# Kernel tuning notes

Measured on AMD Instinct MI355X. Metric: run time of the kernel, lower is better.

## Reference

```python
import jax, jax.numpy as jnp
import numpy as np

G, S, F, H, C, L = 32, 2048, 128, 128, 40, 3
N = G * S           # 65536 nodes
E = N * 16          # 1048576 edges


def setup_inputs() -> dict:
    key = jax.random.key(0)
    ks = jax.random.split(key, 10)
    x = jax.random.normal(ks[0], (N, F), dtype=jnp.float32)
    edge_index = jax.random.randint(ks[1], (2, E), 0, N, dtype=jnp.int64)
    E_meta = jax.random.normal(ks[2], (G, H), dtype=jnp.float32)
    ptr = (jnp.arange(G + 1, dtype=jnp.int64) * S)  # uniform partitions
    # learned params (xavier-ish scaling)
    w0 = jax.random.normal(ks[3], (F, 1), dtype=jnp.float32) * (2.0 / (F + 1)) ** 0.5
    b0 = jax.random.normal(ks[4], (F, H), dtype=jnp.float32) * (2.0 / (F + H)) ** 0.5
    conv_w = jax.random.normal(ks[5], (L, H, H), dtype=jnp.float32) * (1.0 / H) ** 0.5
    conv_b = jnp.zeros((L, H), dtype=jnp.float32)
    lt1_w = jax.random.normal(ks[6], (C, H), dtype=jnp.float32) * (1.0 / H) ** 0.5
    lt1_b = jnp.zeros((C,), dtype=jnp.float32)
    return {"x": x, "edge_index": edge_index, "E_meta": E_meta, "ptr": ptr,
            "w0": w0, "b0": b0, "conv_w": conv_w, "conv_b": conv_b,
            "lt1_w": lt1_w, "lt1_b": lt1_b}


def _gcn_conv(h, src, dst, deg_inv_sqrt, W, b):
    # GCNConv (PyG defaults): h' = D^-1/2 (A+I) D^-1/2 (h W) + b
    hw = h @ W                                          # [N,H]
    norm = deg_inv_sqrt[src] * deg_inv_sqrt[dst]        # [E+N]
    msg = hw[src] * norm[:, None]                       # gather + scale
    return jax.ops.segment_sum(msg, dst, num_segments=h.shape[0]) + b


def reference(x, edge_index, E_meta, ptr, w0, b0, conv_w, conv_b, lt1_w, lt1_b):
    n_nodes = x.shape[0]
    g = E_meta.shape[0]
    s = n_nodes // g  # uniform ptr (ptr[i] = i*s) by construction
    # per-partition dynamic weight: relu(w0 @ emb^T + b0) -> [G,F,H]
    Wdyn = jax.nn.relu(w0[None, :, :] * E_meta[:, None, :] + b0[None, :, :])
    # segment matmul x[ptr[i]:ptr[i+1]] @ Wdyn[i], concatenated -> [N,H]
    h = jnp.einsum('gsf,gfh->gsh', x.reshape(g, s, -1), Wdyn).reshape(n_nodes, -1)
    # add self loops once; symmetric normalization on target degree
    loop = jnp.arange(n_nodes, dtype=edge_index.dtype)
    src = jnp.concatenate([edge_index[0], loop])
    dst = jnp.concatenate([edge_index[1], loop])
    deg = jax.ops.segment_sum(jnp.ones_like(dst, dtype=h.dtype), dst,
                              num_segments=n_nodes)
    deg_inv_sqrt = jnp.where(deg > 0, jax.lax.rsqrt(deg), 0.0)
    for l in range(conv_w.shape[0]):
        h = jax.nn.relu(_gcn_conv(h, src, dst, deg_inv_sqrt, conv_w[l], conv_b[l]))
        # F.dropout with training=False is identity (eval mode)
    logits = h @ lt1_w.T + lt1_b
    return jax.nn.log_softmax(logits, axis=1)
```

## Files before the change

### kernel.cpp

```cpp
#include <hip/hip_runtime.h>

#define NNODES 65536
#define NEDGES 1048576
#define HDIM 128
#define NCLS 40
#define BCAP 6144

#define FP8_SCALE 32.0f
#define FP8_INV   0.03125f

typedef unsigned int uint;
typedef __attribute__((ext_vector_type(8))) short bf16x8;
typedef __attribute__((ext_vector_type(4))) float f32x4;
typedef __attribute__((ext_vector_type(2))) float f32x2;

__device__ __forceinline__ float bf_lo(uint v) {
    return __builtin_bit_cast(float, v << 16);
}
__device__ __forceinline__ float bf_hi(uint v) {
    return __builtin_bit_cast(float, v & 0xffff0000u);
}
__device__ __forceinline__ uint pack_bf16x2(float a, float b) {
    uint ua = __builtin_bit_cast(uint, a);
    uint ub = __builtin_bit_cast(uint, b);
    ua += 0x7fff + ((ua >> 16) & 1);
    ub += 0x7fff + ((ub >> 16) & 1);
    return (ua >> 16) | (ub & 0xffff0000u);
}
__device__ __forceinline__ float tobf(float v) {
    uint u = __builtin_bit_cast(uint, v);
    u += 0x7fff + ((u >> 16) & 1);
    return __builtin_bit_cast(float, u & 0xffff0000u);
}

__device__ __forceinline__ f32x2 fp8_pair(uint u) {
    return __builtin_amdgcn_cvt_pk_f32_fp8((int)u, false);
}

__global__ __launch_bounds__(256) void convT_kernel(
    const float* __restrict__ cw, uint* __restrict__ WT, int* __restrict__ gcursor,
    const float* __restrict__ ltw, uint* __restrict__ WcT8)
{
    int t = threadIdx.x;
    if (blockIdx.x == 0) gcursor[t] = 0;
    int idx = blockIdx.x * 256 + t;
    if (idx < 24576) {
        int ip = idx & 63;
        int o = (idx >> 6) & 127;
        int l = idx >> 13;
        int i0 = ip * 2;
        float v0 = cw[l * 16384 + i0 * 128 + o];
        float v1 = cw[l * 16384 + (i0 + 1) * 128 + o];
        WT[idx] = pack_bf16x2(v0, v1);
    } else {
        int idx2 = idx - 24576;
        int part = (idx2 >= 3072) ? 1 : 0;
        int r = idx2 - part * 3072;
        int o = r >> 6;
        int ip = r & 63;
        float v0 = 0.f, v1 = 0.f;
        if (o < NCLS) {
            float w0v = ltw[o * 128 + ip * 2];
            float w1v = ltw[o * 128 + ip * 2 + 1];
            float h0 = tobf(w0v), h1 = tobf(w1v);
            if (part == 0) { v0 = h0; v1 = h1; }
            else { v0 = w0v - h0; v1 = w1v - h1; }
        }
        WcT8[idx2] = pack_bf16x2(v0, v1);
    }
}

__global__ __launch_bounds__(256) void bucket_scatter(
    const int* __restrict__ src, const int* __restrict__ dst,
    int* __restrict__ gcursor, uint* __restrict__ binned)
{
    __shared__ int lcnt[256];
    __shared__ int lbase[256];
    int t = threadIdx.x;
    int base = blockIdx.x * 4096;
    lcnt[t] = 0;
    __syncthreads();
    uint e[16];
#pragma unroll
    for (int k = 0; k < 16; k++) {
        int i = base + k * 256 + t;
        uint s = (uint)src[i];
        uint d = (uint)dst[i];
        e[k] = (d << 16) | s;
        atomicAdd(&lcnt[d >> 8], 1);
    }
    __syncthreads();
    lbase[t] = t * BCAP + atomicAdd(&gcursor[t], lcnt[t]);
    lcnt[t] = 0;
    __syncthreads();
#pragma unroll
    for (int k = 0; k < 16; k++) {
        int b = e[k] >> 24;
        int r = atomicAdd(&lcnt[b], 1);
        binned[lbase[b] + r] = e[k];
    }
}

__global__ __launch_bounds__(256) void prep_kernel(
    const uint* __restrict__ binned, const int* __restrict__ gcursor,
    int* __restrict__ row_beg, int* __restrict__ row_end4,
    float* __restrict__ dis, int* __restrict__ csr,
    const float* __restrict__ w0, const float* __restrict__ em,
    const float* __restrict__ b0, const uint* __restrict__ convwT0,
    uint* __restrict__ WT)
{
    __shared__ int cnt[256];
    __shared__ int tmp[256];
    __shared__ int fb[256];
    const int t = threadIdx.x;

    if (blockIdx.x < 256) {
        int b = blockIdx.x;
        int e0 = b * BCAP, e1 = e0 + gcursor[b];
        cnt[t] = 0;
        __syncthreads();
        for (int i = e0 + t; i < e1; i += 256)
            atomicAdd(&cnt[(binned[i] >> 16) & 255], 1);
        __syncthreads();
        int v = cnt[t];
        int size4 = (v + 3) & ~3;
        tmp[t] = size4;
        __syncthreads();
        for (int off = 1; off < 256; off <<= 1) {
            int u = (t >= off) ? tmp[t - off] : 0;
            __syncthreads();
            tmp[t] += u;
            __syncthreads();
        }
        fb[t] = tmp[t] - size4;
        int node = (b << 8) + t;
        int beg = e0 + fb[t];
        row_beg[node] = beg;
        row_end4[node] = beg + size4;
        dis[node] = rsqrtf((float)(v + 1));
        for (int p = v; p < size4; p++) csr[beg + p] = NNODES;
        cnt[t] = 0;
        __syncthreads();
        for (int i = e0 + t; i < e1; i += 256) {
            uint e = binned[i];
            int d = (e >> 16) & 255;
            int r = atomicAdd(&cnt[d], 1);
            csr[e0 + fb[d] + r] = (int)(e & 0xffffu);
        }
    } else {
        int bb = blockIdx.x - 256;
        const int g = bb >> 3;
        const int c = bb & 7;
        const int wave = t >> 6;
        const int lane = t & 63;
        const int q = lane >> 4;
        const int l16 = lane & 15;
        const float* emg = em + g * 128;

        f32x4 acc[2];
#pragma unroll
        for (int r = 0; r < 2; r++) {
            acc[r][0] = 0.f; acc[r][1] = 0.f; acc[r][2] = 0.f; acc[r][3] = 0.f;
        }
        const int f = c * 16 + l16;
        const float wf = w0[f];

#pragma unroll
        for (int k0 = 0; k0 < 128; k0 += 32) {
            const int kf = k0 + q * 8;
            bf16x8 afrag[2];
#pragma unroll
            for (int r = 0; r < 2; r++) {
                uint4 u = *(const uint4*)(convwT0 +
                    (size_t)(wave * 32 + r * 16 + l16) * 64 + (kf >> 1));
                afrag[r] = __builtin_bit_cast(bf16x8, u);
            }
            float4 e0 = *(const float4*)(emg + kf);
            float4 e1 = *(const float4*)(emg + kf + 4);
            const float* bp = b0 + (size_t)f * 128 + kf;
            float4 bb0 = *(const float4*)bp;
            float4 bb1 = *(const float4*)(bp + 4);
            float v0 = fmaxf(fmaf(wf, e0.x, bb0.x), 0.f);
            float v1 = fmaxf(fmaf(wf, e0.y, bb0.y), 0.f);
            float v2 = fmaxf(fmaf(wf, e0.z, bb0.z), 0.f);
            float v3 = fmaxf(fmaf(wf, e0.w, bb0.w), 0.f);
            float v4 = fmaxf(fmaf(wf, e1.x, bb1.x), 0.f);
            float v5 = fmaxf(fmaf(wf, e1.y, bb1.y), 0.f);
            float v6 = fmaxf(fmaf(wf, e1.z, bb1.z), 0.f);
            float v7 = fmaxf(fmaf(wf, e1.w, bb1.w), 0.f);
            uint4 u;
            u.x = pack_bf16x2(v0, v1);
            u.y = pack_bf16x2(v2, v3);
            u.z = pack_bf16x2(v4, v5);
            u.w = pack_bf16x2(v6, v7);
            bf16x8 bfrag = __builtin_bit_cast(bf16x8, u);
#pragma unroll
            for (int r = 0; r < 2; r++)
                acc[r] = __builtin_amdgcn_mfma_f32_16x16x32_bf16(
                    afrag[r], bfrag, acc[r], 0, 0, 0);
        }

        uint* WTg = WT + (size_t)g * 8192;
#pragma unroll
        for (int r = 0; r < 2; r++) {
            int o0 = wave * 32 + r * 16 + q * 4;
#pragma unroll
            for (int i = 0; i < 4; i++) {
                int o = o0 + i;
                float v = acc[r][i];
                float w = __shfl_xor(v, 1);
                uint p = (lane & 1) ? pack_bf16x2(w, v) : pack_bf16x2(v, w);
                if (!(lane & 1))
                    WTg[(size_t)o * 64 + (uint)(f >> 1)] = p;
            }
        }
    }
}

__device__ __forceinline__ void store_fp8_row(
    uint* __restrict__ Cp8, int row, float s32, const f32x4* accRC,
    int lane, int l16, int i)
{
#pragma unroll
    for (int c = 0; c < 8; c++) {
        float v = accRC[c][i] * s32;
        float w = __shfl_xor(v, 1);
        int us = __builtin_amdgcn_cvt_pk_fp8_f32(v, w, 0, false);
        uint partner = (uint)__shfl_xor(us, 2);
        if ((lane & 3) == 0) {
            uint p = ((uint)us & 0xffffu) | (partner << 16);
            Cp8[(size_t)row * 32 + c * 4 + (l16 >> 2)] = p;
        }
    }
}

__global__ __launch_bounds__(256) void gemm_mfma(
    const float* __restrict__ A, const uint* __restrict__ BT,
    uint* __restrict__ Cp8, const float* __restrict__ dis, int perGroup)
{
    const int t = threadIdx.x;
    const int wave = t >> 6;
    const int lane = t & 63;
    const int q = lane >> 4;
    const int l16 = lane & 15;
    const int rowBase = blockIdx.x * 128;
    const uint* Bp = perGroup ? BT + ((size_t)(rowBase >> 11) << 13) : BT;

    if (blockIdx.x == 0 && t < 32)
        Cp8[(size_t)NNODES * 32 + t] = 0u;

    f32x4 acc[2][8];
#pragma unroll
    for (int r = 0; r < 2; r++)
#pragma unroll
        for (int c = 0; c < 8; c++) {
            acc[r][c][0] = 0.f; acc[r][c][1] = 0.f;
            acc[r][c][2] = 0.f; acc[r][c][3] = 0.f;
        }

    const int mBase = rowBase + wave * 32 + l16;

#pragma unroll
    for (int k0 = 0; k0 < 128; k0 += 32) {
        const int kf = k0 + q * 8;
        bf16x8 afrag[2];
#pragma unroll
        for (int r = 0; r < 2; r++) {
            const float* ap = A + (size_t)(mBase + r * 16) * 128 + kf;
            float4 a0 = *(const float4*)ap;
            float4 a1 = *(const float4*)(ap + 4);
            uint4 u;
            u.x = pack_bf16x2(a0.x, a0.y);
            u.y = pack_bf16x2(a0.z, a0.w);
            u.z = pack_bf16x2(a1.x, a1.y);
            u.w = pack_bf16x2(a1.z, a1.w);
            afrag[r] = __builtin_bit_cast(bf16x8, u);
        }
#pragma unroll
        for (int c = 0; c < 8; c++) {
            uint4 u = *(const uint4*)(Bp + (size_t)(c * 16 + l16) * 64 + (kf >> 1));
            bf16x8 bfrag = __builtin_bit_cast(bf16x8, u);
#pragma unroll
            for (int r = 0; r < 2; r++)
                acc[r][c] = __builtin_amdgcn_mfma_f32_16x16x32_bf16(
                    afrag[r], bfrag, acc[r][c], 0, 0, 0);
        }
    }

#pragma unroll
    for (int r = 0; r < 2; r++) {
        int row0 = rowBase + wave * 32 + r * 16 + q * 4;
#pragma unroll
        for (int i = 0; i < 4; i++) {
            int row = row0 + i;
            float s32 = dis[row] * FP8_SCALE;
            store_fp8_row(Cp8, row, s32, acc[r], lane, l16, i);
        }
    }
}

__device__ __forceinline__ void aggregate_eighth(
    const uint* __restrict__ hws8_in, const int* __restrict__ row_beg,
    const int* __restrict__ row_end4, const int* __restrict__ csr,
    const float* __restrict__ dis, const float* __restrict__ bias,
    uint* __restrict__ hT, int rowBase, int wave, int lane)
{
    const int g = lane >> 3;
    const int s = lane & 7;
    const int nl = wave * 8 + g;
    const int n = rowBase + nl;
    const int beg = row_beg[n];
    const int end4 = row_end4[n];
    int mx = (end4 - beg) >> 2;
    mx = max(mx, __shfl_xor(mx, 8));
    mx = max(mx, __shfl_xor(mx, 16));
    mx = max(mx, __shfl_xor(mx, 32));

    uint4 su = *((const uint4*)(hws8_in + (size_t)n * 32) + s);
    f32x2 a[8];
    a[0] = fp8_pair(su.x); a[1] = fp8_pair(su.x >> 16);
    a[2] = fp8_pair(su.y); a[3] = fp8_pair(su.y >> 16);
    a[4] = fp8_pair(su.z); a[5] = fp8_pair(su.z >> 16);
    a[6] = fp8_pair(su.w); a[7] = fp8_pair(su.w >> 16);

#define ACC8(u) do { \
        a[0] += fp8_pair((u).x); a[1] += fp8_pair((u).x >> 16); \
        a[2] += fp8_pair((u).y); a[3] += fp8_pair((u).y >> 16); \
        a[4] += fp8_pair((u).z); a[5] += fp8_pair((u).z >> 16); \
        a[6] += fp8_pair((u).w); a[7] += fp8_pair((u).w >> 16); } while (0)

    int i = beg;
    for (int it = 0; it < mx; it += 2, i += 8) {
        int4 sA = *(const int4*)(csr + i);
        int4 sB = *(const int4*)(csr + i + 4);
        if (i >= end4) { sA.x = NNODES; sA.y = NNODES; sA.z = NNODES; sA.w = NNODES; }
        if (i + 4 >= end4) { sB.x = NNODES; sB.y = NNODES; sB.z = NNODES; sB.w = NNODES; }
        uint4 u0 = *((const uint4*)(hws8_in + (size_t)sA.x * 32) + s);
        uint4 u1 = *((const uint4*)(hws8_in + (size_t)sA.y * 32) + s);
        uint4 u2 = *((const uint4*)(hws8_in + (size_t)sA.z * 32) + s);
        uint4 u3 = *((const uint4*)(hws8_in + (size_t)sA.w * 32) + s);
        uint4 u4 = *((const uint4*)(hws8_in + (size_t)sB.x * 32) + s);
        uint4 u5 = *((const uint4*)(hws8_in + (size_t)sB.y * 32) + s);
        uint4 u6 = *((const uint4*)(hws8_in + (size_t)sB.z * 32) + s);
        uint4 u7 = *((const uint4*)(hws8_in + (size_t)sB.w * 32) + s);
        ACC8(u0); ACC8(u1); ACC8(u2); ACC8(u3);
        ACC8(u4); ACC8(u5); ACC8(u6); ACC8(u7);
    }
#undef ACC8

    const float d = dis[n] * FP8_INV;
    const float* bp = bias + s * 16;
    float4 b0 = *(const float4*)bp;
    float4 b1 = *(const float4*)(bp + 4);
    float4 b2 = *(const float4*)(bp + 8);
    float4 b3 = *(const float4*)(bp + 12);
    float o0  = fmaxf(fmaf(d, a[0].x, b0.x), 0.f);
    float o1  = fmaxf(fmaf(d, a[0].y, b0.y), 0.f);
    float o2  = fmaxf(fmaf(d, a[1].x, b0.z), 0.f);
    float o3  = fmaxf(fmaf(d, a[1].y, b0.w), 0.f);
    float o4  = fmaxf(fmaf(d, a[2].x, b1.x), 0.f);
    float o5  = fmaxf(fmaf(d, a[2].y, b1.y), 0.f);
    float o6  = fmaxf(fmaf(d, a[3].x, b1.z), 0.f);
    float o7  = fmaxf(fmaf(d, a[3].y, b1.w), 0.f);
    float o8  = fmaxf(fmaf(d, a[4].x, b2.x), 0.f);
    float o9  = fmaxf(fmaf(d, a[4].y, b2.y), 0.f);
    float o10 = fmaxf(fmaf(d, a[5].x, b2.z), 0.f);
    float o11 = fmaxf(fmaf(d, a[5].y, b2.w), 0.f);
    float o12 = fmaxf(fmaf(d, a[6].x, b3.x), 0.f);
    float o13 = fmaxf(fmaf(d, a[6].y, b3.y), 0.f);
    float o14 = fmaxf(fmaf(d, a[7].x, b3.z), 0.f);
    float o15 = fmaxf(fmaf(d, a[7].y, b3.w), 0.f);
    uint4 w0, w1;
    w0.x = pack_bf16x2(o0, o1);
    w0.y = pack_bf16x2(o2, o3);
    w0.z = pack_bf16x2(o4, o5);
    w0.w = pack_bf16x2(o6, o7);
    w1.x = pack_bf16x2(o8, o9);
    w1.y = pack_bf16x2(o10, o11);
    w1.z = pack_bf16x2(o12, o13);
    w1.w = pack_bf16x2(o14, o15);
    *(uint4*)&hT[nl * 68 + s * 8] = w0;
    *(uint4*)&hT[nl * 68 + s * 8 + 4] = w1;
}

__global__ __launch_bounds__(512) void agg_gemm_kernel(
    const uint* __restrict__ hws8_in, const int* __restrict__ row_beg,
    const int* __restrict__ row_end4, const int* __restrict__ csr,
    const float* __restrict__ dis, const float* __restrict__ bias,
    const uint* __restrict__ BT, uint* __restrict__ out8)
{
    __shared__ uint hT[64 * 68];
    const int t = threadIdx.x;
    const int wave = t >> 6;
    const int lane = t & 63;
    const int rowBase = blockIdx.x * 64;

    if (blockIdx.x == 0 && t < 32)
        out8[(size_t)NNODES * 32 + t] = 0u;

    aggregate_eighth(hws8_in, row_beg, row_end4, csr, dis, bias,
                     hT, rowBase, wave, lane);
    __syncthreads();

    const int q = lane >> 4;
    const int l16 = lane & 15;
    const int mw = wave & 1;
    const int nw = wave >> 1;

    f32x4 acc[2][2];
#pragma unroll
    for (int r = 0; r < 2; r++)
#pragma unroll
        for (int c = 0; c < 2; c++) {
            acc[r][c][0] = 0.f; acc[r][c][1] = 0.f;
            acc[r][c][2] = 0.f; acc[r][c][3] = 0.f;
        }

#pragma unroll
    for (int k0 = 0; k0 < 128; k0 += 32) {
        const int kp = (k0 >> 1) + q * 4;
        bf16x8 afrag[2];
#pragma unroll
        for (int r = 0; r < 2; r++) {
            uint4 u = *(const uint4*)&hT[(mw * 32 + r * 16 + l16) * 68 + kp];
            afrag[r] = __builtin_bit_cast(bf16x8, u);
        }
#pragma unroll
        for (int c = 0; c < 2; c++) {
            uint4 u = *(const uint4*)(BT +
                (size_t)(nw * 32 + c * 16 + l16) * 64 + kp);
            bf16x8 bfrag = __builtin_bit_cast(bf16x8, u);
#pragma unroll
            for (int r = 0; r < 2; r++)
                acc[r][c] = __builtin_amdgcn_mfma_f32_16x16x32_bf16(
                    afrag[r], bfrag, acc[r][c], 0, 0, 0);
        }
    }

#pragma unroll
    for (int r = 0; r < 2; r++) {
        int row0 = rowBase + mw * 32 + r * 16 + q * 4;
#pragma unroll
        for (int i = 0; i < 4; i++) {
            int row = row0 + i;
            float s32 = dis[row] * FP8_SCALE;
#pragma unroll
            for (int c = 0; c < 2; c++) {
                float v = acc[r][c][i] * s32;
                float w = __shfl_xor(v, 1);
                int us = __builtin_amdgcn_cvt_pk_fp8_f32(v, w, 0, false);
                uint partner = (uint)__shfl_xor(us, 2);
                if ((lane & 3) == 0) {
                    uint p = ((uint)us & 0xffffu) | (partner << 16);
                    out8[(size_t)row * 32 + (nw * 2 + c) * 4 + (l16 >> 2)] = p;
                }
            }
        }
    }
}

__global__ __launch_bounds__(512) void agg_logits_kernel(
    const uint* __restrict__ hws8_in, const int* __restrict__ row_beg,
    const int* __restrict__ row_end4, const int* __restrict__ csr,
    const float* __restrict__ dis, const float* __restrict__ bias,
    const uint* __restrict__ WcT8, const float* __restrict__ bc,
    float* __restrict__ out)
{
    __shared__ uint hT[64 * 68];
    const int t = threadIdx.x;
    const int wave = t >> 6;
    const int lane = t & 63;
    const int rowBase = blockIdx.x * 64;

    aggregate_eighth(hws8_in, row_beg, row_end4, csr, dis, bias,
                     hT, rowBase, wave, lane);
    __syncthreads();

    if (wave >= 4) return;

    const int q = lane >> 4;
    const int l16 = lane & 15;

    f32x4 acc[3];
#pragma unroll
    for (int c = 0; c < 3; c++) {
        acc[c][0] = 0.f; acc[c][1] = 0.f; acc[c][2] = 0.f; acc[c][3] = 0.f;
    }

#pragma unroll
    for (int k0 = 0; k0 < 128; k0 += 32) {
        const int kp = (k0 >> 1) + q * 4;
        uint4 ua = *(const uint4*)&hT[(wave * 16 + l16) * 68 + kp];
        bf16x8 af = __builtin_bit_cast(bf16x8, ua);
#pragma unroll
        for (int tile = 0; tile < 3; tile++) {
            uint4 uh = *(const uint4*)(WcT8 + (size_t)(tile * 16 + l16) * 64 + kp);
            uint4 ul = *(const uint4*)(WcT8 + (size_t)(48 + tile * 16 + l16) * 64 + kp);
            acc[tile] = __builtin_amdgcn_mfma_f32_16x16x32_bf16(
                af, __builtin_bit_cast(bf16x8, uh), acc[tile], 0, 0, 0);
            acc[tile] = __builtin_amdgcn_mfma_f32_16x16x32_bf16(
                af, __builtin_bit_cast(bf16x8, ul), acc[tile], 0, 0, 0);
        }
    }

    const float bt0 = bc[l16];
    const float bt1 = bc[16 + l16];
    const float bt2 = (l16 < 8) ? bc[32 + l16] : 0.f;

#pragma unroll
    for (int i = 0; i < 4; i++) {
        const int node = rowBase + wave * 16 + q * 4 + i;
        float g0 = acc[0][i] + bt0;
        float g1 = acc[1][i] + bt1;
        float g2 = (l16 < 8) ? (acc[2][i] + bt2) : -1e30f;
        float m = fmaxf(fmaxf(g0, g1), g2);
        for (int off = 1; off < 16; off <<= 1) m = fmaxf(m, __shfl_xor(m, off));
        float sum = expf(g0 - m) + expf(g1 - m) + ((l16 < 8) ? expf(g2 - m) : 0.f);
        for (int off = 1; off < 16; off <<= 1) sum += __shfl_xor(sum, off);
        float lse = m + logf(sum);
        float* on = out + (size_t)node * NCLS;
        on[l16] = g0 - lse;
        on[16 + l16] = g1 - lse;
        if (l16 < 8) on[32 + l16] = g2 - lse;
    }
}

extern "C" void kernel_launch(void* const* d_in, const int* in_sizes, int n_in,
                              void* d_out, int out_size, void* d_ws, size_t ws_size,
                              hipStream_t stream)
{
    const float* x     = (const float*)d_in[0];
    const int*   ei    = (const int*)d_in[1];
    const float* em    = (const float*)d_in[2];
    const float* w0    = (const float*)d_in[4];
    const float* b0    = (const float*)d_in[5];
    const float* convw = (const float*)d_in[6];
    const float* convb = (const float*)d_in[7];
    const float* ltw   = (const float*)d_in[8];
    const float* ltb   = (const float*)d_in[9];
    float* out = (float*)d_out;

    char* ws = (char*)d_ws;
    size_t off = 0;
    auto alloc = [&](size_t bytes) -> void* {
        void* p = ws + off;
        off += (bytes + 255) & ~(size_t)255;
        return p;
    };
    uint*  hws8A    = (uint*)alloc((size_t)(NNODES + 1) * 32 * 4);
    uint*  hws8B    = (uint*)alloc((size_t)(NNODES + 1) * 32 * 4);
    uint*  WcombT   = (uint*)alloc((size_t)32 * 128 * 64 * 4);
    uint*  convwT   = (uint*)alloc((size_t)3 * 128 * 64 * 4);
    uint*  WcT8     = (uint*)alloc((size_t)96 * 64 * 4);
    int*   gcursor  = (int*)alloc(256 * 4);
    uint*  binned   = (uint*)alloc((size_t)256 * BCAP * 4);
    int*   row_beg  = (int*)alloc((size_t)NNODES * 4);
    int*   row_end4 = (int*)alloc((size_t)NNODES * 4);
    float* dis      = (float*)alloc((size_t)NNODES * 4);
    int*   csr      = (int*)alloc((size_t)256 * BCAP * 4);

    const int* esrc = ei;
    const int* edst = ei + NEDGES;

    convT_kernel<<<120, 256, 0, stream>>>(convw, convwT, gcursor, ltw, WcT8);
    bucket_scatter<<<NEDGES / 4096, 256, 0, stream>>>(esrc, edst, gcursor, binned);
    prep_kernel<<<512, 256, 0, stream>>>(binned, gcursor, row_beg, row_end4, dis,
                                         csr, w0, em, b0, convwT, WcombT);

    gemm_mfma<<<NNODES / 128, 256, 0, stream>>>(x, WcombT, hws8A, dis, 1);

    agg_gemm_kernel<<<NNODES / 64, 512, 0, stream>>>(
        hws8A, row_beg, row_end4, csr, dis, convb + 0 * 128,
        convwT + (size_t)1 * 8192, hws8B);
    agg_gemm_kernel<<<NNODES / 64, 512, 0, stream>>>(
        hws8B, row_beg, row_end4, csr, dis, convb + 1 * 128,
        convwT + (size_t)2 * 8192, hws8A);
    agg_logits_kernel<<<NNODES / 64, 512, 0, stream>>>(
        hws8A, row_beg, row_end4, csr, dis, convb + 2 * 128, WcT8, ltb, out);
}
```

Measured before the change: 240.6 us.

## Fuse graph build and all GCN layers into one persistent kernel with grid barriers

Replaces the chain of bucket-scatter, prep, GEMM and three aggregation kernels with a single persistent 512-block kernel. The stages are separated by a software grid barrier built from an atomic counter plus spin-wait, and a small init kernel packs weights and resets the counters. The goal is to remove launch gaps and pipeline drain between the seven dependent launches. In exchange it depends on all 512 blocks being co-resident: the barrier has a spin cap that silently breaks out, which could cause races or hangs if residency fails. It also adds spin overhead and may lose some load balance.

```diff
diff --git a/kernel.cpp b/kernel.cpp
--- a/kernel.cpp
+++ b/kernel.cpp
@@ -2,24 +2,20 @@
 
 #define NNODES 65536
 #define NEDGES 1048576
-#define HDIM 128
 #define NCLS 40
 #define BCAP 6144
 
 #define FP8_SCALE 32.0f
 #define FP8_INV   0.03125f
+
+#define GRID 512
+#define TPB  512
 
 typedef unsigned int uint;
 typedef __attribute__((ext_vector_type(8))) short bf16x8;
 typedef __attribute__((ext_vector_type(4))) float f32x4;
 typedef __attribute__((ext_vector_type(2))) float f32x2;
 
-__device__ __forceinline__ float bf_lo(uint v) {
-    return __builtin_bit_cast(float, v << 16);
-}
-__device__ __forceinline__ float bf_hi(uint v) {
-    return __builtin_bit_cast(float, v & 0xffff0000u);
-}
 __device__ __forceinline__ uint pack_bf16x2(float a, float b) {
     uint ua = __builtin_bit_cast(uint, a);
     uint ub = __builtin_bit_cast(uint, b);
@@ -32,270 +28,88 @@
     u += 0x7fff + ((u >> 16) & 1);
     return __builtin_bit_cast(float, u & 0xffff0000u);
 }
-
 __device__ __forceinline__ f32x2 fp8_pair(uint u) {
     return __builtin_amdgcn_cvt_pk_f32_fp8((int)u, false);
 }
 
-__global__ __launch_bounds__(256) void convT_kernel(
-    const float* __restrict__ cw, uint* __restrict__ WT, int* __restrict__ gcursor,
-    const float* __restrict__ ltw, uint* __restrict__ WcT8)
+struct Prm {
+    const float* x;
+    const int*   esrc;
+    const int*   edst;
+    const float* em;
+    const float* w0;
+    const float* b0;
+    const float* convw;
+    const float* convb;
+    const float* ltw;
+    const float* ltb;
+    float*       out;
+    uint*  hws8A;
+    uint*  hws8B;
+    uint*  WcombT;
+    uint*  convwT;
+    uint*  WcT8;
+    int*   gcursor;
+    uint*  binned;
+    int*   row_beg;
+    int*   row_end4;
+    float* dis;
+    int*   csr;
+    int*   bar;
+};
+
+__device__ __forceinline__ void gridbar(int* bar, int target, int t) {
+    __syncthreads();
+    if (t == 0) {
+        __hip_atomic_fetch_add(bar, 1, __ATOMIC_RELEASE, __HIP_MEMORY_SCOPE_AGENT);
+        int spins = 0;
+        while (__hip_atomic_load(bar, __ATOMIC_RELAXED,
+                                 __HIP_MEMORY_SCOPE_AGENT) < target) {
+            __builtin_amdgcn_s_sleep(8);
+            if (++spins > (1 << 20)) break;
+        }
+        __threadfence();
+    }
+    __syncthreads();
+}
+
+__global__ __launch_bounds__(256) void init_pack(Prm p)
 {
     int t = threadIdx.x;
-    if (blockIdx.x == 0) gcursor[t] = 0;
-    int idx = blockIdx.x * 256 + t;
-    if (idx < 24576) {
-        int ip = idx & 63;
-        int o = (idx >> 6) & 127;
-        int l = idx >> 13;
-        int i0 = ip * 2;
-        float v0 = cw[l * 16384 + i0 * 128 + o];
-        float v1 = cw[l * 16384 + (i0 + 1) * 128 + o];
-        WT[idx] = pack_bf16x2(v0, v1);
-    } else {
-        int idx2 = idx - 24576;
-        int part = (idx2 >= 3072) ? 1 : 0;
-        int r = idx2 - part * 3072;
-        int o = r >> 6;
-        int ip = r & 63;
-        float v0 = 0.f, v1 = 0.f;
-        if (o < NCLS) {
-            float w0v = ltw[o * 128 + ip * 2];
-            float w1v = ltw[o * 128 + ip * 2 + 1];
-            float h0 = tobf(w0v), h1 = tobf(w1v);
-            if (part == 0) { v0 = h0; v1 = h1; }
-            else { v0 = w0v - h0; v1 = w1v - h1; }
-        }
-        WcT8[idx2] = pack_bf16x2(v0, v1);
-    }
-}
-
-__global__ __launch_bounds__(256) void bucket_scatter(
-    const int* __restrict__ src, const int* __restrict__ dst,
-    int* __restrict__ gcursor, uint* __restrict__ binned)
-{
-    __shared__ int lcnt[256];
-    __shared__ int lbase[256];
-    int t = threadIdx.x;
-    int base = blockIdx.x * 4096;
-    lcnt[t] = 0;
-    __syncthreads();
-    uint e[16];
-#pragma unroll
-    for (int k = 0; k < 16; k++) {
-        int i = base + k * 256 + t;
-        uint s = (uint)src[i];
-        uint d = (uint)dst[i];
-        e[k] = (d << 16) | s;
-        atomicAdd(&lcnt[d >> 8], 1);
-    }
-    __syncthreads();
-    lbase[t] = t * BCAP + atomicAdd(&gcursor[t], lcnt[t]);
-    lcnt[t] = 0;
-    __syncthreads();
-#pragma unroll
-    for (int k = 0; k < 16; k++) {
-        int b = e[k] >> 24;
-        int r = atomicAdd(&lcnt[b], 1);
-        binned[lbase[b] + r] = e[k];
-    }
-}
-
-__global__ __launch_bounds__(256) void prep_kernel(
-    const uint* __restrict__ binned, const int* __restrict__ gcursor,
-    int* __restrict__ row_beg, int* __restrict__ row_end4,
-    float* __restrict__ dis, int* __restrict__ csr,
-    const float* __restrict__ w0, const float* __restrict__ em,
-    const float* __restrict__ b0, const uint* __restrict__ convwT0,
-    uint* __restrict__ WT)
-{
-    __shared__ int cnt[256];
-    __shared__ int tmp[256];
-    __shared__ int fb[256];
-    const int t = threadIdx.x;
-
-    if (blockIdx.x < 256) {
-        int b = blockIdx.x;
-        int e0 = b * BCAP, e1 = e0 + gcursor[b];
-        cnt[t] = 0;
-        __syncthreads();
-        for (int i = e0 + t; i < e1; i += 256)
-            atomicAdd(&cnt[(binned[i] >> 16) & 255], 1);
-        __syncthreads();
-        int v = cnt[t];
-        int size4 = (v + 3) & ~3;
-        tmp[t] = size4;
-        __syncthreads();
-        for (int off = 1; off < 256; off <<= 1) {
-            int u = (t >= off) ? tmp[t - off] : 0;
-            __syncthreads();
-            tmp[t] += u;
-            __syncthreads();
-        }
-        fb[t] = tmp[t] - size4;
-        int node = (b << 8) + t;
-        int beg = e0 + fb[t];
-        row_beg[node] = beg;
-        row_end4[node] = beg + size4;
-        dis[node] = rsqrtf((float)(v + 1));
-        for (int p = v; p < size4; p++) csr[beg + p] = NNODES;
-        cnt[t] = 0;
-        __syncthreads();
-        for (int i = e0 + t; i < e1; i += 256) {
-            uint e = binned[i];
-            int d = (e >> 16) & 255;
-            int r = atomicAdd(&cnt[d], 1);
-            csr[e0 + fb[d] + r] = (int)(e & 0xffffu);
-        }
-    } else {
-        int bb = blockIdx.x - 256;
-        const int g = bb >> 3;
-        const int c = bb & 7;
-        const int wave = t >> 6;
-        const int lane = t & 63;
-        const int q = lane >> 4;
-        const int l16 = lane & 15;
-        const float* emg = em + g * 128;
-
-        f32x4 acc[2];
-#pragma unroll
-        for (int r = 0; r < 2; r++) {
-            acc[r][0] = 0.f; acc[r][1] = 0.f; acc[r][2] = 0.f; acc[r][3] = 0.f;
-        }
-        const int f = c * 16 + l16;
-        const float wf = w0[f];
-
-#pragma unroll
-        for (int k0 = 0; k0 < 128; k0 += 32) {
-            const int kf = k0 + q * 8;
-            bf16x8 afrag[2];
-#pragma unroll
-            for (int r = 0; r < 2; r++) {
-                uint4 u = *(const uint4*)(convwT0 +
-                    (size_t)(wave * 32 + r * 16 + l16) * 64 + (kf >> 1));
-                afrag[r] = __builtin_bit_cast(bf16x8, u);
-            }
-            float4 e0 = *(const float4*)(emg + kf);
-            float4 e1 = *(const float4*)(emg + kf + 4);
-            const float* bp = b0 + (size_t)f * 128 + kf;
-            float4 bb0 = *(const float4*)bp;
-            float4 bb1 = *(const float4*)(bp + 4);
-            float v0 = fmaxf(fmaf(wf, e0.x, bb0.x), 0.f);
-            float v1 = fmaxf(fmaf(wf, e0.y, bb0.y), 0.f);
-            float v2 = fmaxf(fmaf(wf, e0.z, bb0.z), 0.f);
-            float v3 = fmaxf(fmaf(wf, e0.w, bb0.w), 0.f);
-            float v4 = fmaxf(fmaf(wf, e1.x, bb1.x), 0.f);
-            float v5 = fmaxf(fmaf(wf, e1.y, bb1.y), 0.f);
-            float v6 = fmaxf(fmaf(wf, e1.z, bb1.z), 0.f);
-            float v7 = fmaxf(fmaf(wf, e1.w, bb1.w), 0.f);
-            uint4 u;
-            u.x = pack_bf16x2(v0, v1);
-            u.y = pack_bf16x2(v2, v3);
-            u.z = pack_bf16x2(v4, v5);
-            u.w = pack_bf16x2(v6, v7);
-            bf16x8 bfrag = __builtin_bit_cast(bf16x8, u);
-#pragma unroll
-            for (int r = 0; r < 2; r++)
-                acc[r] = __builtin_amdgcn_mfma_f32_16x16x32_bf16(
-                    afrag[r], bfrag, acc[r], 0, 0, 0);
-        }
-
-        uint* WTg = WT + (size_t)g * 8192;
-#pragma unroll
-        for (int r = 0; r < 2; r++) {
-            int o0 = wave * 32 + r * 16 + q * 4;
-#pragma unroll
-            for (int i = 0; i < 4; i++) {
-                int o = o0 + i;
-                float v = acc[r][i];
-                float w = __shfl_xor(v, 1);
-                uint p = (lane & 1) ? pack_bf16x2(w, v) : pack_bf16x2(v, w);
-                if (!(lane & 1))
-                    WTg[(size_t)o * 64 + (uint)(f >> 1)] = p;
-            }
-        }
-    }
-}
-
-__device__ __forceinline__ void store_fp8_row(
-    uint* __restrict__ Cp8, int row, float s32, const f32x4* accRC,
-    int lane, int l16, int i)
-{
-#pragma unroll
-    for (int c = 0; c < 8; c++) {
-        float v = accRC[c][i] * s32;
-        float w = __shfl_xor(v, 1);
-        int us = __builtin_amdgcn_cvt_pk_fp8_f32(v, w, 0, false);
-        uint partner = (uint)__shfl_xor(us, 2);
-        if ((lane & 3) == 0) {
-            uint p = ((uint)us & 0xffffu) | (partner << 16);
-            Cp8[(size_t)row * 32 + c * 4 + (l16 >> 2)] = p;
-        }
-    }
-}
-
-__global__ __launch_bounds__(256) void gemm_mfma(
-    const float* __restrict__ A, const uint* __restrict__ BT,
-    uint* __restrict__ Cp8, const float* __restrict__ dis, int perGroup)
-{
-    const int t = threadIdx.x;
-    const int wave = t >> 6;
-    const int lane = t & 63;
-    const int q = lane >> 4;
-    const int l16 = lane & 15;
-    const int rowBase = blockIdx.x * 128;
-    const uint* Bp = perGroup ? BT + ((size_t)(rowBase >> 11) << 13) : BT;
-
-    if (blockIdx.x == 0 && t < 32)
-        Cp8[(size_t)NNODES * 32 + t] = 0u;
-
-    f32x4 acc[2][8];
-#pragma unroll
-    for (int r = 0; r < 2; r++)
-#pragma unroll
-        for (int c = 0; c < 8; c++) {
-            acc[r][c][0] = 0.f; acc[r][c][1] = 0.f;
-            acc[r][c][2] = 0.f; acc[r][c][3] = 0.f;
-        }
-
-    const int mBase = rowBase + wave * 32 + l16;
-
-#pragma unroll
-    for (int k0 = 0; k0 < 128; k0 += 32) {
-        const int kf = k0 + q * 8;
-        bf16x8 afrag[2];
-#pragma unroll
-        for (int r = 0; r < 2; r++) {
-            const float* ap = A + (size_t)(mBase + r * 16) * 128 + kf;
-            float4 a0 = *(const float4*)ap;
-            float4 a1 = *(const float4*)(ap + 4);
-            uint4 u;
-            u.x = pack_bf16x2(a0.x, a0.y);
-            u.y = pack_bf16x2(a0.z, a0.w);
-            u.z = pack_bf16x2(a1.x, a1.y);
-            u.w = pack_bf16x2(a1.z, a1.w);
-            afrag[r] = __builtin_bit_cast(bf16x8, u);
-        }
-#pragma unroll
-        for (int c = 0; c < 8; c++) {
-            uint4 u = *(const uint4*)(Bp + (size_t)(c * 16 + l16) * 64 + (kf >> 1));
-            bf16x8 bfrag = __builtin_bit_cast(bf16x8, u);
-#pragma unroll
-            for (int r = 0; r < 2; r++)
-                acc[r][c] = __builtin_amdgcn_mfma_f32_16x16x32_bf16(
-                    afrag[r], bfrag, acc[r][c], 0, 0, 0);
-        }
-    }
-
-#pragma unroll
-    for (int r = 0; r < 2; r++) {
-        int row0 = rowBase + wave * 32 + r * 16 + q * 4;
-#pragma unroll
-        for (int i = 0; i < 4; i++) {
-            int row = row0 + i;
-            float s32 = dis[row] * FP8_SCALE;
-            store_fp8_row(Cp8, row, s32, acc[r], lane, l16, i);
-        }
+    int b = blockIdx.x;
+    for (int idx = b * 256 + t; idx < 30720; idx += 120 * 256) {
+        if (idx < 24576) {
+            int ip = idx & 63;
+            int o = (idx >> 6) & 127;
+            int l = idx >> 13;
+            int i0 = ip * 2;
+            float v0 = p.convw[l * 16384 + i0 * 128 + o];
+            float v1 = p.convw[l * 16384 + (i0 + 1) * 128 + o];
+            p.convwT[idx] = pack_bf16x2(v0, v1);
+        } else {
+            int idx2 = idx - 24576;
+            int part = (idx2 >= 3072) ? 1 : 0;
+            int r = idx2 - part * 3072;
+            int o = r >> 6;
+            int ip = r & 63;
+            float v0 = 0.f, v1 = 0.f;
+            if (o < NCLS) {
+                float w0v = p.ltw[o * 128 + ip * 2];
+                float w1v = p.ltw[o * 128 + ip * 2 + 1];
+                float h0 = tobf(w0v), h1 = tobf(w1v);
+                if (part == 0) { v0 = h0; v1 = h1; }
+                else { v0 = w0v - h0; v1 = w1v - h1; }
+            }
+            p.WcT8[idx2] = pack_bf16x2(v0, v1);
+        }
+    }
+    if (b == 0) {
+        p.gcursor[t] = 0;
+        if (t < 16) p.bar[t] = 0;
+    }
+    if (b == 1 && t < 64) {
+        if (t < 32) p.hws8A[(size_t)NNODES * 32 + t] = 0u;
+        else        p.hws8B[(size_t)NNODES * 32 + (t - 32)] = 0u;
     }
 }
 
@@ -383,25 +197,11 @@
     *(uint4*)&hT[nl * 68 + s * 8 + 4] = w1;
 }
 
-__global__ __launch_bounds__(512) void agg_gemm_kernel(
-    const uint* __restrict__ hws8_in, const int* __restrict__ row_beg,
-    const int* __restrict__ row_end4, const int* __restrict__ csr,
-    const float* __restrict__ dis, const float* __restrict__ bias,
-    const uint* __restrict__ BT, uint* __restrict__ out8)
+__device__ __forceinline__ void gemm64(
+    const uint* __restrict__ hT, const uint* __restrict__ BT,
+    const float* __restrict__ dis, uint* __restrict__ out8,
+    int rowBase, int wave, int lane)
 {
-    __shared__ uint hT[64 * 68];
-    const int t = threadIdx.x;
-    const int wave = t >> 6;
-    const int lane = t & 63;
-    const int rowBase = blockIdx.x * 64;
-
-    if (blockIdx.x == 0 && t < 32)
-        out8[(size_t)NNODES * 32 + t] = 0u;
-
-    aggregate_eighth(hws8_in, row_beg, row_end4, csr, dis, bias,
-                     hT, rowBase, wave, lane);
-    __syncthreads();
-
     const int q = lane >> 4;
     const int l16 = lane & 15;
     const int mw = wave & 1;
@@ -451,77 +251,310 @@
                 int us = __builtin_amdgcn_cvt_pk_fp8_f32(v, w, 0, false);
                 uint partner = (uint)__shfl_xor(us, 2);
                 if ((lane & 3) == 0) {
-                    uint p = ((uint)us & 0xffffu) | (partner << 16);
-                    out8[(size_t)row * 32 + (nw * 2 + c) * 4 + (l16 >> 2)] = p;
+                    uint pk = ((uint)us & 0xffffu) | (partner << 16);
+                    out8[(size_t)row * 32 + (nw * 2 + c) * 4 + (l16 >> 2)] = pk;
                 }
             }
         }
     }
 }
 
-__global__ __launch_bounds__(512) void agg_logits_kernel(
-    const uint* __restrict__ hws8_in, const int* __restrict__ row_beg,
-    const int* __restrict__ row_end4, const int* __restrict__ csr,
-    const float* __restrict__ dis, const float* __restrict__ bias,
-    const uint* __restrict__ WcT8, const float* __restrict__ bc,
-    float* __restrict__ out)
+__global__ __launch_bounds__(TPB, 4) void gnn_mono(Prm p)
 {
-    __shared__ uint hT[64 * 68];
+    __shared__ __align__(16) char smem[64 * 68 * 4];
+    const int bid = blockIdx.x;
     const int t = threadIdx.x;
     const int wave = t >> 6;
     const int lane = t & 63;
-    const int rowBase = blockIdx.x * 64;
-
-    aggregate_eighth(hws8_in, row_beg, row_end4, csr, dis, bias,
-                     hT, rowBase, wave, lane);
-    __syncthreads();
-
-    if (wave >= 4) return;
-
-    const int q = lane >> 4;
-    const int l16 = lane & 15;
-
-    f32x4 acc[3];
-#pragma unroll
-    for (int c = 0; c < 3; c++) {
-        acc[c][0] = 0.f; acc[c][1] = 0.f; acc[c][2] = 0.f; acc[c][3] = 0.f;
-    }
-
-#pragma unroll
-    for (int k0 = 0; k0 < 128; k0 += 32) {
-        const int kp = (k0 >> 1) + q * 4;
-        uint4 ua = *(const uint4*)&hT[(wave * 16 + l16) * 68 + kp];
-        bf16x8 af = __builtin_bit_cast(bf16x8, ua);
-#pragma unroll
-        for (int tile = 0; tile < 3; tile++) {
-            uint4 uh = *(const uint4*)(WcT8 + (size_t)(tile * 16 + l16) * 64 + kp);
-            uint4 ul = *(const uint4*)(WcT8 + (size_t)(48 + tile * 16 + l16) * 64 + kp);
-            acc[tile] = __builtin_amdgcn_mfma_f32_16x16x32_bf16(
-                af, __builtin_bit_cast(bf16x8, uh), acc[tile], 0, 0, 0);
-            acc[tile] = __builtin_amdgcn_mfma_f32_16x16x32_bf16(
-                af, __builtin_bit_cast(bf16x8, ul), acc[tile], 0, 0, 0);
-        }
-    }
-
-    const float bt0 = bc[l16];
-    const float bt1 = bc[16 + l16];
-    const float bt2 = (l16 < 8) ? bc[32 + l16] : 0.f;
-
-#pragma unroll
-    for (int i = 0; i < 4; i++) {
-        const int node = rowBase + wave * 16 + q * 4 + i;
-        float g0 = acc[0][i] + bt0;
-        float g1 = acc[1][i] + bt1;
-        float g2 = (l16 < 8) ? (acc[2][i] + bt2) : -1e30f;
-        float m = fmaxf(fmaxf(g0, g1), g2);
-        for (int off = 1; off < 16; off <<= 1) m = fmaxf(m, __shfl_xor(m, off));
-        float sum = expf(g0 - m) + expf(g1 - m) + ((l16 < 8) ? expf(g2 - m) : 0.f);
-        for (int off = 1; off < 16; off <<= 1) sum += __shfl_xor(sum, off);
-        float lse = m + logf(sum);
-        float* on = out + (size_t)node * NCLS;
-        on[l16] = g0 - lse;
-        on[16 + l16] = g1 - lse;
-        if (l16 < 8) on[32 + l16] = g2 - lse;
+
+    {
+        int* lcnt = (int*)smem;
+        int* lbase = lcnt + 256;
+        int base = bid * 2048;
+        if (t < 256) lcnt[t] = 0;
+        __syncthreads();
+        uint e[4];
+#pragma unroll
+        for (int k = 0; k < 4; k++) {
+            int i = base + k * 512 + t;
+            uint s = (uint)p.esrc[i];
+            uint d = (uint)p.edst[i];
+            e[k] = (d << 16) | s;
+            atomicAdd(&lcnt[d >> 8], 1);
+        }
+        __syncthreads();
+        if (t < 256) {
+            lbase[t] = t * BCAP + atomicAdd(&p.gcursor[t], lcnt[t]);
+            lcnt[t] = 0;
+        }
+        __syncthreads();
+#pragma unroll
+        for (int k = 0; k < 4; k++) {
+            int b = e[k] >> 24;
+            int r = atomicAdd(&lcnt[b], 1);
+            p.binned[lbase[b] + r] = e[k];
+        }
+    }
+    gridbar(p.bar, 1 * GRID, t);
+
+    if (bid < 256) {
+        int* cnt = (int*)smem;
+        int* tmp = cnt + 256;
+        int* fb = tmp + 256;
+        int b = bid;
+        int e0 = b * BCAP, e1 = e0 + p.gcursor[b];
+        if (t < 256) cnt[t] = 0;
+        __syncthreads();
+        for (int i = e0 + t; i < e1; i += 512)
+            atomicAdd(&cnt[(p.binned[i] >> 16) & 255], 1);
+        __syncthreads();
+        int v = 0, size4 = 0;
+        if (t < 256) {
+            v = cnt[t];
+            size4 = (v + 3) & ~3;
+            tmp[t] = size4;
+        }
+        __syncthreads();
+        for (int off = 1; off < 256; off <<= 1) {
+            int u = (t >= off && t < 256) ? tmp[t - off] : 0;
+            __syncthreads();
+            if (t < 256) tmp[t] += u;
+            __syncthreads();
+        }
+        if (t < 256) {
+            fb[t] = tmp[t] - size4;
+            int node = (b << 8) + t;
+            int beg = e0 + fb[t];
+            p.row_beg[node] = beg;
+            p.row_end4[node] = beg + size4;
+            p.dis[node] = rsqrtf((float)(v + 1));
+            for (int q2 = v; q2 < size4; q2++) p.csr[beg + q2] = NNODES;
+            cnt[t] = 0;
+        }
+        __syncthreads();
+        for (int i = e0 + t; i < e1; i += 512) {
+            uint e = p.binned[i];
+            int d = (e >> 16) & 255;
+            int r = atomicAdd(&cnt[d], 1);
+            p.csr[e0 + fb[d] + r] = (int)(e & 0xffffu);
+        }
+    } else if (wave < 4) {
+        int bb = bid - 256;
+        const int g = bb >> 3;
+        const int c = bb & 7;
+        const int q = lane >> 4;
+        const int l16 = lane & 15;
+        const float* emg = p.em + g * 128;
+
+        f32x4 acc[2];
+#pragma unroll
+        for (int r = 0; r < 2; r++) {
+            acc[r][0] = 0.f; acc[r][1] = 0.f; acc[r][2] = 0.f; acc[r][3] = 0.f;
+        }
+        const int f = c * 16 + l16;
+        const float wf = p.w0[f];
+
+#pragma unroll
+        for (int k0 = 0; k0 < 128; k0 += 32) {
+            const int kf = k0 + q * 8;
+            bf16x8 afrag[2];
+#pragma unroll
+            for (int r = 0; r < 2; r++) {
+                uint4 u = *(const uint4*)(p.convwT +
+                    (size_t)(wave * 32 + r * 16 + l16) * 64 + (kf >> 1));
+                afrag[r] = __builtin_bit_cast(bf16x8, u);
+            }
+            float4 e0 = *(const float4*)(emg + kf);
+            float4 e1 = *(const float4*)(emg + kf + 4);
+            const float* bp = p.b0 + (size_t)f * 128 + kf;
+            float4 bb0 = *(const float4*)bp;
+            float4 bb1 = *(const float4*)(bp + 4);
+            float v0 = fmaxf(fmaf(wf, e0.x, bb0.x), 0.f);
+            float v1 = fmaxf(fmaf(wf, e0.y, bb0.y), 0.f);
+            float v2 = fmaxf(fmaf(wf, e0.z, bb0.z), 0.f);
+            float v3 = fmaxf(fmaf(wf, e0.w, bb0.w), 0.f);
+            float v4 = fmaxf(fmaf(wf, e1.x, bb1.x), 0.f);
+            float v5 = fmaxf(fmaf(wf, e1.y, bb1.y), 0.f);
+            float v6 = fmaxf(fmaf(wf, e1.z, bb1.z), 0.f);
+            float v7 = fmaxf(fmaf(wf, e1.w, bb1.w), 0.f);
+            uint4 u;
+            u.x = pack_bf16x2(v0, v1);
+            u.y = pack_bf16x2(v2, v3);
+            u.z = pack_bf16x2(v4, v5);
+            u.w = pack_bf16x2(v6, v7);
+            bf16x8 bfrag = __builtin_bit_cast(bf16x8, u);
+#pragma unroll
+            for (int r = 0; r < 2; r++)
+                acc[r] = __builtin_amdgcn_mfma_f32_16x16x32_bf16(
+                    afrag[r], bfrag, acc[r], 0, 0, 0);
+        }
+
+        uint* WTg = p.WcombT + (size_t)g * 8192;
+#pragma unroll
+        for (int r = 0; r < 2; r++) {
+            int o0 = wave * 32 + r * 16 + q * 4;
+#pragma unroll
+            for (int i = 0; i < 4; i++) {
+                int o = o0 + i;
+                float v = acc[r][i];
+                float w = __shfl_xor(v, 1);
+                uint pk = (lane & 1) ? pack_bf16x2(w, v) : pack_bf16x2(v, w);
+                if (!(lane & 1))
+                    WTg[(size_t)o * 64 + (uint)(f >> 1)] = pk;
+            }
+        }
+    }
+    gridbar(p.bar, 2 * GRID, t);
+
+    {
+        const int q = lane >> 4;
+        const int l16 = lane & 15;
+        const int rowBase = bid * 128;
+        const int mw = wave & 3;
+        const int nw = wave >> 2;
+        const uint* Bp = p.WcombT + ((size_t)(rowBase >> 11) << 13);
+
+        f32x4 acc[2][4];
+#pragma unroll
+        for (int r = 0; r < 2; r++)
+#pragma unroll
+            for (int c = 0; c < 4; c++) {
+                acc[r][c][0] = 0.f; acc[r][c][1] = 0.f;
+                acc[r][c][2] = 0.f; acc[r][c][3] = 0.f;
+            }
+
+        const int mBase = rowBase + mw * 32 + l16;
+
+#pragma unroll
+        for (int k0 = 0; k0 < 128; k0 += 32) {
+            const int kf = k0 + q * 8;
+            bf16x8 afrag[2];
+#pragma unroll
+            for (int r = 0; r < 2; r++) {
+                const float* ap = p.x + (size_t)(mBase + r * 16) * 128 + kf;
+                float4 a0 = *(const float4*)ap;
+                float4 a1 = *(const float4*)(ap + 4);
+                uint4 u;
+                u.x = pack_bf16x2(a0.x, a0.y);
+                u.y = pack_bf16x2(a0.z, a0.w);
+                u.z = pack_bf16x2(a1.x, a1.y);
+                u.w = pack_bf16x2(a1.z, a1.w);
+                afrag[r] = __builtin_bit_cast(bf16x8, u);
+            }
+#pragma unroll
+            for (int c = 0; c < 4; c++) {
+                uint4 u = *(const uint4*)(Bp +
+                    (size_t)(nw * 64 + c * 16 + l16) * 64 + (kf >> 1));
+                bf16x8 bfrag = __builtin_bit_cast(bf16x8, u);
+#pragma unroll
+                for (int r = 0; r < 2; r++)
+                    acc[r][c] = __builtin_amdgcn_mfma_f32_16x16x32_bf16(
+                        afrag[r], bfrag, acc[r][c], 0, 0, 0);
+            }
+        }
+
+#pragma unroll
+        for (int r = 0; r < 2; r++) {
+            int row0 = rowBase + mw * 32 + r * 16 + q * 4;
+#pragma unroll
+            for (int i = 0; i < 4; i++) {
+                int row = row0 + i;
+                float s32 = p.dis[row] * FP8_SCALE;
+#pragma unroll
+                for (int c = 0; c < 4; c++) {
+                    float v = acc[r][c][i] * s32;
+                    float w = __shfl_xor(v, 1);
+                    int us = __builtin_amdgcn_cvt_pk_fp8_f32(v, w, 0, false);
+                    uint partner = (uint)__shfl_xor(us, 2);
+                    if ((lane & 3) == 0) {
+                        uint pk = ((uint)us & 0xffffu) | (partner << 16);
+                        p.hws8A[(size_t)row * 32 + nw * 16 + c * 4 + (l16 >> 2)] = pk;
+                    }
+                }
+            }
+        }
+    }
+    gridbar(p.bar, 3 * GRID, t);
+
+    uint* hT = (uint*)smem;
+#pragma unroll 1
+    for (int layer = 0; layer < 2; layer++) {
+        const uint* in8 = layer ? p.hws8B : p.hws8A;
+        uint* out8 = layer ? p.hws8A : p.hws8B;
+        const uint* BT = p.convwT + (size_t)(layer + 1) * 8192;
+        const float* bias = p.convb + layer * 128;
+#pragma unroll 1
+        for (int vt = bid; vt < NNODES / 64; vt += GRID) {
+            const int rowBase = vt * 64;
+            aggregate_eighth(in8, p.row_beg, p.row_end4, p.csr, p.dis, bias,
+                             hT, rowBase, wave, lane);
+            __syncthreads();
+            gemm64(hT, BT, p.dis, out8, rowBase, wave, lane);
+            __syncthreads();
+        }
+        gridbar(p.bar, (4 + layer) * GRID, t);
+    }
+
+#pragma unroll 1
+    for (int vt = bid; vt < NNODES / 64; vt += GRID) {
+        const int rowBase = vt * 64;
+        aggregate_eighth(p.hws8A, p.row_beg, p.row_end4, p.csr, p.dis,
+                         p.convb + 2 * 128, hT, rowBase, wave, lane);
+        __syncthreads();
+
+        if (wave < 4) {
+            const int q = lane >> 4;
+            const int l16 = lane & 15;
+
+            f32x4 acc[3];
+#pragma unroll
+            for (int c = 0; c < 3; c++) {
+                acc[c][0] = 0.f; acc[c][1] = 0.f; acc[c][2] = 0.f; acc[c][3] = 0.f;
+            }
+
+#pragma unroll
+            for (int k0 = 0; k0 < 128; k0 += 32) {
+                const int kp = (k0 >> 1) + q * 4;
+                uint4 ua = *(const uint4*)&hT[(wave * 16 + l16) * 68 + kp];
+                bf16x8 af = __builtin_bit_cast(bf16x8, ua);
+#pragma unroll
+                for (int tile = 0; tile < 3; tile++) {
+                    uint4 uh = *(const uint4*)(p.WcT8 +
+                        (size_t)(tile * 16 + l16) * 64 + kp);
+                    uint4 ul = *(const uint4*)(p.WcT8 +
+                        (size_t)(48 + tile * 16 + l16) * 64 + kp);
+                    acc[tile] = __builtin_amdgcn_mfma_f32_16x16x32_bf16(
+                        af, __builtin_bit_cast(bf16x8, uh), acc[tile], 0, 0, 0);
+                    acc[tile] = __builtin_amdgcn_mfma_f32_16x16x32_bf16(
+                        af, __builtin_bit_cast(bf16x8, ul), acc[tile], 0, 0, 0);
+                }
+            }
+
+            const float bt0 = p.ltb[l16];
+            const float bt1 = p.ltb[16 + l16];
+            const float bt2 = (l16 < 8) ? p.ltb[32 + l16] : 0.f;
+
+#pragma unroll
+            for (int i = 0; i < 4; i++) {
+                const int node = rowBase + wave * 16 + q * 4 + i;
+                float g0 = acc[0][i] + bt0;
+                float g1 = acc[1][i] + bt1;
+                float g2 = (l16 < 8) ? (acc[2][i] + bt2) : -1e30f;
+                float m = fmaxf(fmaxf(g0, g1), g2);
+                for (int off = 1; off < 16; off <<= 1)
+                    m = fmaxf(m, __shfl_xor(m, off));
+                float sum = expf(g0 - m) + expf(g1 - m) +
+                            ((l16 < 8) ? expf(g2 - m) : 0.f);
+                for (int off = 1; off < 16; off <<= 1)
+                    sum += __shfl_xor(sum, off);
+                float lse = m + logf(sum);
+                float* on = p.out + (size_t)node * NCLS;
+                on[l16] = g0 - lse;
+                on[16 + l16] = g1 - lse;
+                if (l16 < 8) on[32 + l16] = g2 - lse;
+            }
+        }
+        __syncthreads();
     }
 }
 
@@ -529,52 +562,40 @@
                               void* d_out, int out_size, void* d_ws, size_t ws_size,
                               hipStream_t stream)
 {
-    const float* x     = (const float*)d_in[0];
-    const int*   ei    = (const int*)d_in[1];
-    const float* em    = (const float*)d_in[2];
-    const float* w0    = (const float*)d_in[4];
-    const float* b0    = (const float*)d_in[5];
-    const float* convw = (const float*)d_in[6];
-    const float* convb = (const float*)d_in[7];
-    const float* ltw   = (const float*)d_in[8];
-    const float* ltb   = (const float*)d_in[9];
-    float* out = (float*)d_out;
+    Prm p;
+    p.x     = (const float*)d_in[0];
+    const int* ei = (const int*)d_in[1];
+    p.em    = (const float*)d_in[2];
+    p.w0    = (const float*)d_in[4];
+    p.b0    = (const float*)d_in[5];
+    p.convw = (const float*)d_in[6];
+    p.convb = (const float*)d_in[7];
+    p.ltw   = (const float*)d_in[8];
+    p.ltb   = (const float*)d_in[9];
+    p.out   = (float*)d_out;
+    p.esrc  = ei;
+    p.edst  = ei + NEDGES;
 
     char* ws = (char*)d_ws;
     size_t off = 0;
     auto alloc = [&](size_t bytes) -> void* {
-        void* p = ws + off;
+        void* q = ws + off;
         off += (bytes + 255) & ~(size_t)255;
-        return p;
+        return q;
     };
-    uint*  hws8A    = (uint*)alloc((size_t)(NNODES + 1) * 32 * 4);
-    uint*  hws8B    = (uint*)alloc((size_t)(NNODES + 1) * 32 * 4);
-    uint*  WcombT   = (uint*)alloc((size_t)32 * 128 * 64 * 4);
-    uint*  convwT   = (uint*)alloc((size_t)3 * 128 * 64 * 4);
-    uint*  WcT8     = (uint*)alloc((size_t)96 * 64 * 4);
-    int*   gcursor  = (int*)alloc(256 * 4);
-    uint*  binned   = (uint*)alloc((size_t)256 * BCAP * 4);
-    int*   row_beg  = (int*)alloc((size_t)NNODES * 4);
-    int*   row_end4 = (int*)alloc((size_t)NNODES * 4);
-    float* dis      = (float*)alloc((size_t)NNODES * 4);
-    int*   csr      = (int*)alloc((size_t)256 * BCAP * 4);
-
-    const int* esrc = ei;
-    const int* edst = ei + NEDGES;
-
-    convT_kernel<<<120, 256, 0, stream>>>(convw, convwT, gcursor, ltw, WcT8);
-    bucket_scatter<<<NEDGES / 4096, 256, 0, stream>>>(esrc, edst, gcursor, binned);
-    prep_kernel<<<512, 256, 0, stream>>>(binned, gcursor, row_beg, row_end4, dis,
-                                         csr, w0, em, b0, convwT, WcombT);
-
-    gemm_mfma<<<NNODES / 128, 256, 0, stream>>>(x, WcombT, hws8A, dis, 1);
-
-    agg_gemm_kernel<<<NNODES / 64, 512, 0, stream>>>(
-        hws8A, row_beg, row_end4, csr, dis, convb + 0 * 128,
-        convwT + (size_t)1 * 8192, hws8B);
-    agg_gemm_kernel<<<NNODES / 64, 512, 0, stream>>>(
-        hws8B, row_beg, row_end4, csr, dis, convb + 1 * 128,
-        convwT + (size_t)2 * 8192, hws8A);
-    agg_logits_kernel<<<NNODES / 64, 512, 0, stream>>>(
-        hws8A, row_beg, row_end4, csr, dis, convb + 2 * 128, WcT8, ltb, out);
-}
+    p.hws8A    = (uint*)alloc((size_t)(NNODES + 1) * 32 * 4);
+    p.hws8B    = (uint*)alloc((size_t)(NNODES + 1) * 32 * 4);
+    p.WcombT   = (uint*)alloc((size_t)32 * 128 * 64 * 4);
+    p.convwT   = (uint*)alloc((size_t)3 * 128 * 64 * 4);
+    p.WcT8     = (uint*)alloc((size_t)96 * 64 * 4);
+    p.gcursor  = (int*)alloc(256 * 4);
+    p.binned   = (uint*)alloc((size_t)256 * BCAP * 4);
+    p.row_beg  = (int*)alloc((size_t)NNODES * 4);
+    p.row_end4 = (int*)alloc((size_t)NNODES * 4);
+    p.dis      = (float*)alloc((size_t)NNODES * 4);
+    p.csr      = (int*)alloc((size_t)256 * BCAP * 4);
+    p.bar      = (int*)alloc(256 * 4);
+
+    init_pack<<<120, 256, 0, stream>>>(p);
+    gnn_mono<<<GRID, TPB, 0, stream>>>(p);
+}
```

Measured after the change: 501.5 us. 2.08x slower.
